# Performance work log

Measured on AMD Instinct MI355X. Metric: run time of the kernel, lower is better.

Reference implementation:

```python
import jax, jax.numpy as jnp
import numpy as np

BETA_HAT_2 = 2.0


def _forward(x, cw0, cb0, cw1, cb1, cw2, cb2,
             Wq, bq, Wk, bk, Wv, bv, Wo, bo, omega, gamma, W1, b1, W2, b2):
    # ---- conv frontal stem: (Conv1D same -> ReLU -> AvgPool(4)) x 3 ----
    def conv_relu(h, w, b):
        y = jax.lax.conv_general_dilated(h, w, window_strides=(1,), padding='SAME',
                                         dimension_numbers=('NWC', 'WIO', 'NWC'))
        return jax.nn.relu(y + b)

    def avg_pool(h, p=4):
        B, L, C = h.shape
        return h.reshape(B, L // p, p, C).mean(axis=2)

    h = avg_pool(conv_relu(x, cw0, cb0))
    h = avg_pool(conv_relu(h, cw1, cb1))
    h = avg_pool(conv_relu(h, cw2, cb2))   # [B, S, D]

    B, S, D = h.shape
    H, Dh = gamma.shape[1], omega.shape[2]
    M = 2 * omega.shape[3]                 # d_kernel_map
    inv_sqrt_m = 1.0 / np.sqrt(M)

    # ---- PositionalFeature: normalized positions x ALiBi-like slope ladder ----
    slopes = jnp.arange(D, 0, -4.0, dtype=h.dtype) / D * BETA_HAT_2   # [D/4]
    t = jnp.arange(S, dtype=h.dtype) / (S - 1)                        # [S]
    fwd = t[:, None] * slopes[None, :]                                # [S, D/4]
    pos_q = jnp.concatenate([fwd, fwd[::-1]], axis=-1)                # [S, M] (forward, backward)
    pos_k = -pos_q                                                    # (neg_forward, neg_backward)

    def lc(z):  # LayerCentering: mean-subtraction over features (no scale)
        return z - z.mean(axis=-1, keepdims=True)

    def fourier(z, om):  # z [B,S,H,Dh], om [H,Dh,M/2] -> [B,S,H,M]
        proj = jnp.einsum('bshd,hdm->bshm', z, om)
        return jnp.concatenate([jnp.cos(proj), jnp.sin(proj)], axis=-1) * inv_sqrt_m

    def layer(carry, p):
        hc = carry
        wq, bq_, wk, bk_, wv, bv_, wo, bo_, om, g, w1, b1_, w2, b2_ = p
        a_in = lc(hc)  # preLC
        q = (a_in @ wq + bq_).reshape(B, S, H, Dh)
        k = (a_in @ wk + bk_).reshape(B, S, H, Dh)
        v = (a_in @ wv + bv_).reshape(B, S, H, Dh)
        qf = fourier(q, om)
        kf = fourier(k, om)
        # factorized exponential positional modulation, per-head learnable slope g:
        # A_ij[m] ~ qf_i[m] kf_j[m] exp(g*s_m*(t_i - t_j))  (ALiBi-style, linear-time)
        eq = jnp.exp(g[None, :, None] * pos_q[:, None, :])  # [S,H,M]
        ek = jnp.exp(g[None, :, None] * pos_k[:, None, :])  # [S,H,M]
        qt = qf * eq[None]
        kt = kf * ek[None]
        kv = jnp.einsum('bshm,bshe->bhme', kt, v)            # [B,H,M,Dh]
        o = jnp.einsum('bshm,bhme->bshe', qt, kv).reshape(B, S, H * Dh)
        hc = hc + (o @ wo + bo_)                              # residual (dropout inactive)
        f_in = lc(hc)                                         # preLC before FF
        hc = hc + (jax.nn.relu(f_in @ w1 + b1_) @ w2 + b2_)   # PositionwiseFF + residual
        return hc, None

    h, _ = jax.lax.scan(layer, h, (Wq, bq, Wk, bk, Wv, bv, Wo, bo, omega, gamma, W1, b1, W2, b2))
    return h


def setup_inputs() -> dict:
    key = jax.random.key(0)
    ks = jax.random.split(key, 16)
    B, Lraw = 8, 131072
    NL, D, H, Dh, Dff, M = 2, 256, 8, 32, 1024, 128
    f32 = jnp.float32
    x = jax.random.normal(ks[0], (B, Lraw, 1), f32)

    def w(k, shape, fan_in):
        return jax.random.normal(k, shape, f32) / np.sqrt(fan_in)

    cw0 = w(ks[1], (11, 1, 8), 11 * 1)
    cw1 = w(ks[2], (3, 8, 16), 3 * 8)
    cw2 = w(ks[3], (3, 16, D), 3 * 16)
    Wq = w(ks[4], (NL, D, H * Dh), D)
    Wk = w(ks[5], (NL, D, H * Dh), D)
    Wv = w(ks[6], (NL, D, H * Dh), D)
    Wo = w(ks[7], (NL, H * Dh, D), H * Dh)
    W1 = w(ks[8], (NL, D, Dff), D)
    W2 = w(ks[9], (NL, Dff, D), Dff)
    omega = jax.random.normal(ks[10], (NL, H, Dh, M // 2), f32)  # fourier projection
    g0 = jax.random.uniform(ks[11], (1, H), f32, 0.0, 0.5)       # layer 0: head_init_range (0, 0.5)
    gr = jax.random.uniform(ks[12], (NL - 1, H), f32, 0.0, 1.0)  # others: (0, 1.0) ('forward')
    gamma = jnp.concatenate([g0, gr], axis=0)
    z = lambda *s: jnp.zeros(s, f32)
    return {"x": x, "cw0": cw0, "cb0": z(8), "cw1": cw1, "cb1": z(16), "cw2": cw2, "cb2": z(D),
            "Wq": Wq, "bq": z(NL, H * Dh), "Wk": Wk, "bk": z(NL, H * Dh), "Wv": Wv, "bv": z(NL, H * Dh),
            "Wo": Wo, "bo": z(NL, D), "omega": omega, "gamma": gamma,
            "W1": W1, "b1": z(NL, Dff), "W2": W2, "b2": z(NL, D)}


def reference(x, cw0, cb0, cw1, cb1, cw2, cb2, Wq, bq, Wk, bk, Wv, bv, Wo, bo, omega, gamma, W1, b1, W2, b2):
    return _forward(x, cw0, cb0, cw1, cb1, cw2, cb2,
                    Wq, bq, Wk, bk, Wv, bv, Wo, bo, omega, gamma, W1, b1, W2, b2)
```

## Files before the change

kernel.cpp:

```cpp
#include <hip/hip_runtime.h>
#include <hip/hip_bf16.h>
#include <math.h>

#define BATCH 8
#define LRAW 131072
#define L1P 32768
#define L2P 8192
#define SEQ 2048
#define DMODEL 256
#define NHEAD 8
#define DHEAD 32
#define MDIM 128
#define MHALF 64
#define DFF 1024
#define BS_TOK (BATCH*SEQ)
#define INV_SQRT_M 0.08838834764831845f

typedef __attribute__((ext_vector_type(8))) short s8v;
typedef __attribute__((ext_vector_type(4))) float f4v;

static __device__ __forceinline__ f4v mfma16(s8v a, s8v b, f4v c) {
    return __builtin_amdgcn_mfma_f32_16x16x32_bf16(a, b, c, 0, 0, 0);
}
static __device__ __forceinline__ unsigned short f2bf(float x) {
    __hip_bfloat16 h = __float2bfloat16(x);
    return *reinterpret_cast<unsigned short*>(&h);
}
static __device__ __forceinline__ float bf2f(unsigned short u) {
    __hip_bfloat16 h; *reinterpret_cast<unsigned short*>(&h) = u;
    return __bfloat162float(h);
}
static __device__ __forceinline__ void split8(const float* v, unsigned short* dh, unsigned short* dl) {
#pragma unroll
    for (int j = 0; j < 8; j++) {
        unsigned short hv = f2bf(v[j]);
        dh[j] = hv;
        dl[j] = f2bf(v[j] - bf2f(hv));
    }
}
static __device__ __forceinline__ void split_frag(const float* v, s8v& hi, s8v& lo) {
#pragma unroll
    for (int j = 0; j < 8; j++) {
        unsigned short hv = f2bf(v[j]);
        hi[j] = (short)hv;
        lo[j] = (short)f2bf(v[j] - bf2f(hv));
    }
}
static __device__ __forceinline__ int swz(int row, int kq) {
    return row * 32 + ((kq ^ ((row >> 1) & 3)) << 3);
}


__global__ __launch_bounds__(256) void conv0_kernel(const float* __restrict__ x,
    const float* __restrict__ w, const float* __restrict__ bias, float* __restrict__ out)
{
    int idx = blockIdx.x * 256 + threadIdx.x;
    if (idx >= BATCH * L1P) return;
    int b = idx >> 15;
    int p = idx & (L1P - 1);
    const float* xb = x + (size_t)b * LRAW;
    float acc[8];
#pragma unroll
    for (int c = 0; c < 8; c++) acc[c] = 0.f;
#pragma unroll
    for (int i = 0; i < 4; i++) {
        int base = 4 * p + i - 5;
        float y[8];
#pragma unroll
        for (int c = 0; c < 8; c++) y[c] = bias[c];
#pragma unroll
        for (int kk = 0; kk < 11; kk++) {
            int xi = base + kk;
            float xv = (xi >= 0 && xi < LRAW) ? xb[xi] : 0.f;
#pragma unroll
            for (int c = 0; c < 8; c++) y[c] = fmaf(xv, w[kk * 8 + c], y[c]);
        }
#pragma unroll
        for (int c = 0; c < 8; c++) acc[c] += fmaxf(y[c], 0.f);
    }
    float* op = out + (size_t)idx * 8;
#pragma unroll
    for (int c = 0; c < 8; c++) op[c] = acc[c] * 0.25f;
}

__global__ __launch_bounds__(256) void conv1_kernel(const float* __restrict__ in,
    const float* __restrict__ w, const float* __restrict__ bias, float* __restrict__ out)
{
    int idx = blockIdx.x * 256 + threadIdx.x;
    if (idx >= BATCH * L2P) return;
    int b = idx >> 13;
    int p = idx & (L2P - 1);
    const float* ib = in + (size_t)b * L1P * 8;
    float acc[16];
#pragma unroll
    for (int c = 0; c < 16; c++) acc[c] = 0.f;
#pragma unroll
    for (int i = 0; i < 4; i++) {
        float y[16];
#pragma unroll
        for (int c = 0; c < 16; c++) y[c] = bias[c];
#pragma unroll
        for (int kk = 0; kk < 3; kk++) {
            int pos = 4 * p + i + kk - 1;
            if (pos < 0 || pos >= L1P) continue;
            const float* row = ib + (size_t)pos * 8;
#pragma unroll
            for (int ci = 0; ci < 8; ci++) {
                float xv = row[ci];
#pragma unroll
                for (int c = 0; c < 16; c++) y[c] = fmaf(xv, w[(kk * 8 + ci) * 16 + c], y[c]);
            }
        }
#pragma unroll
        for (int c = 0; c < 16; c++) acc[c] += fmaxf(y[c], 0.f);
    }
    float* op = out + (size_t)idx * 16;
#pragma unroll
    for (int c = 0; c < 16; c++) op[c] = acc[c] * 0.25f;
}

__global__ __launch_bounds__(256) void conv2_kernel(const float* __restrict__ in,
    const float* __restrict__ w, const float* __restrict__ bias, float* __restrict__ out)
{
    int bp = blockIdx.x;
    int b = bp / SEQ, p = bp % SEQ;
    int co = threadIdx.x;
    __shared__ float win[6][16];
    int t = threadIdx.x;
    if (t < 96) {
        int r = t / 16, ci = t % 16;
        int pos = 4 * p - 1 + r;
        win[r][ci] = (pos >= 0 && pos < L2P) ? in[((size_t)b * L2P + pos) * 16 + ci] : 0.f;
    }
    __syncthreads();
    float y[4];
#pragma unroll
    for (int i = 0; i < 4; i++) y[i] = bias[co];
#pragma unroll
    for (int kk = 0; kk < 3; kk++) {
#pragma unroll
        for (int ci = 0; ci < 16; ci++) {
            float wv = w[(kk * 16 + ci) * 256 + co];
#pragma unroll
            for (int i = 0; i < 4; i++) y[i] = fmaf(win[i + kk][ci], wv, y[i]);
        }
    }
    float acc = 0.f;
#pragma unroll
    for (int i = 0; i < 4; i++) acc += fmaxf(y[i], 0.f);
    out[((size_t)b * SEQ + p) * 256 + co] = acc * 0.25f;
}


__global__ __launch_bounds__(256) void tconv4_kernel(
    const float* __restrict__ s0, const float* __restrict__ s1,
    const float* __restrict__ s2, const float* __restrict__ s3,
    unsigned short* __restrict__ dst)
{
    int z = blockIdx.z;
    const float* in = (z == 0) ? s0 : (z == 1) ? s1 : (z == 2) ? s2 : s3;
    unsigned short* outs = dst + (size_t)z * 131072;
    const int R = 256, C = 256;
    __shared__ float tile[32][33];
    int t = threadIdx.x;
    int r0 = blockIdx.y * 32, c0 = blockIdx.x * 32;
    int r = t >> 3, cq = t & 7;
    float4 v = *(const float4*)(in + (size_t)(r0 + r) * C + c0 + cq * 4);
    tile[r][cq * 4 + 0] = v.x; tile[r][cq * 4 + 1] = v.y;
    tile[r][cq * 4 + 2] = v.z; tile[r][cq * 4 + 3] = v.w;
    __syncthreads();
    ushort4 hi, lo;
    unsigned short* hp = (unsigned short*)&hi;
    unsigned short* lp = (unsigned short*)&lo;
#pragma unroll
    for (int j = 0; j < 4; j++) {
        float x = tile[cq * 4 + j][r];
        hp[j] = f2bf(x);
        lp[j] = f2bf(x - bf2f(hp[j]));
    }
    size_t ob = (size_t)(c0 + r) * (2 * R) + r0 + cq * 4;
    *(ushort4*)&outs[ob] = hi;
    *(ushort4*)&outs[ob + R] = lo;
}

__global__ __launch_bounds__(256) void tconv_ff_kernel(
    const float* __restrict__ W1_l, const float* __restrict__ W2_l,
    unsigned short* __restrict__ w1t, unsigned short* __restrict__ w2t)
{
    int z = blockIdx.z;
    int bx = z ? blockIdx.y : blockIdx.x;
    int by = z ? blockIdx.x : blockIdx.y;
    const float* in = z ? W2_l : W1_l;
    unsigned short* outs = z ? w2t : w1t;
    int R = z ? 1024 : 256;
    int C = z ? 256 : 1024;
    __shared__ float tile[32][33];
    int t = threadIdx.x;
    int r0 = by * 32, c0 = bx * 32;
    int r = t >> 3, cq = t & 7;
    float4 v = *(const float4*)(in + (size_t)(r0 + r) * C + c0 + cq * 4);
    tile[r][cq * 4 + 0] = v.x; tile[r][cq * 4 + 1] = v.y;
    tile[r][cq * 4 + 2] = v.z; tile[r][cq * 4 + 3] = v.w;
    __syncthreads();
    ushort4 hi, lo;
    unsigned short* hp = (unsigned short*)&hi;
    unsigned short* lp = (unsigned short*)&lo;
#pragma unroll
    for (int j = 0; j < 4; j++) {
        float x = tile[cq * 4 + j][r];
        hp[j] = f2bf(x);
        lp[j] = f2bf(x - bf2f(hp[j]));
    }
    size_t ob = (size_t)(c0 + r) * (2 * R) + r0 + cq * 4;
    *(ushort4*)&outs[ob] = hi;
    *(ushort4*)&outs[ob + R] = lo;
}


__global__ __launch_bounds__(256) void center_split(
    const float* __restrict__ hc, unsigned short* __restrict__ hcs)
{
    __shared__ float psum[64][4];
    __shared__ float muS[64];
    const int t = threadIdx.x;
    const int row = t >> 2, q4 = t & 3;
    const size_t grow = (size_t)blockIdx.x * 64 + row;
    const float* rp = hc + grow * DMODEL + q4 * 64;
    float4 va[16];
    float s = 0.f;
#pragma unroll
    for (int j = 0; j < 16; j++) {
        va[j] = *(const float4*)(rp + j * 4);
        s += va[j].x + va[j].y + va[j].z + va[j].w;
    }
    psum[row][q4] = s;
    __syncthreads();
    if (t < 64) muS[t] = (psum[t][0] + psum[t][1] + psum[t][2] + psum[t][3]) * (1.0f / 256.0f);
    __syncthreads();
    const float mu = muS[row];
    unsigned short* op = hcs + grow * 512 + q4 * 64;
#pragma unroll
    for (int j = 0; j < 8; j++) {
        float v[8] = {va[2*j].x - mu, va[2*j].y - mu, va[2*j].z - mu, va[2*j].w - mu,
                      va[2*j+1].x - mu, va[2*j+1].y - mu, va[2*j+1].z - mu, va[2*j+1].w - mu};
        unsigned short hb[8], lb[8];
        split8(v, hb, lb);
        *(uint4*)(op + j * 8) = *(const uint4*)hb;
        *(uint4*)(op + 256 + j * 8) = *(const uint4*)lb;
    }
}


template<bool RESID>
__global__ __launch_bounds__(256) void gemm64s(
    const unsigned short* __restrict__ Abuf, int ARS, int ALO,
    const unsigned short* __restrict__ Bbuf, int BRS, int BLO,
    const float* __restrict__ bias, const float* __restrict__ resid,
    float* __restrict__ C, int N, int K)
{
    __shared__ unsigned short AsH[64 * 32];
    __shared__ unsigned short AsL[64 * 32];
    __shared__ unsigned short BsH[64 * 32];
    __shared__ unsigned short BsL[64 * 32];
    const int t = threadIdx.x;
    const int n0 = blockIdx.y * 64, m0 = blockIdx.x * 64;
    const int row = t >> 2, kq = t & 3, seg = kq * 8;
    const int lane = t & 63, w = t >> 6;
    const int wm = w & 1, wn = w >> 1, m16 = lane & 15, q = lane >> 4;
    const f4v fz = {0.f, 0.f, 0.f, 0.f};
    f4v acc[2][2] = {{fz, fz}, {fz, fz}};
    const size_t aoff = (size_t)(m0 + row) * ARS + seg;
    const size_t boff = (size_t)(n0 + row) * BRS + seg;
    const int lw = swz(row, kq);
    for (int k0 = 0; k0 < K; k0 += 32) {
        __syncthreads();
        *(uint4*)&AsH[lw] = *(const uint4*)(Abuf + aoff + k0);
        *(uint4*)&AsL[lw] = *(const uint4*)(Abuf + aoff + ALO + k0);
        *(uint4*)&BsH[lw] = *(const uint4*)(Bbuf + boff + k0);
        *(uint4*)&BsL[lw] = *(const uint4*)(Bbuf + boff + BLO + k0);
        __syncthreads();
        s8v ah[2], al[2], bh[2], bl[2];
#pragma unroll
        for (int i = 0; i < 2; i++) {
            int ar = wm * 32 + i * 16 + m16;
            int br = wn * 32 + i * 16 + m16;
            int ro = swz(ar, q);
            int co = swz(br, q);
            ah[i] = *(const s8v*)&AsH[ro];
            al[i] = *(const s8v*)&AsL[ro];
            bh[i] = *(const s8v*)&BsH[co];
            bl[i] = *(const s8v*)&BsL[co];
        }
#pragma unroll
        for (int mt = 0; mt < 2; mt++)
#pragma unroll
            for (int nt = 0; nt < 2; nt++) {
                acc[mt][nt] = mfma16(ah[mt], bh[nt], acc[mt][nt]);
                acc[mt][nt] = mfma16(ah[mt], bl[nt], acc[mt][nt]);
                acc[mt][nt] = mfma16(al[mt], bh[nt], acc[mt][nt]);
            }
    }
#pragma unroll
    for (int mt = 0; mt < 2; mt++)
#pragma unroll
        for (int nt = 0; nt < 2; nt++)
#pragma unroll
            for (int r = 0; r < 4; r++) {
                int rg = m0 + wm * 32 + mt * 16 + q * 4 + r;
                int cg = n0 + wn * 32 + nt * 16 + m16;
                float val = acc[mt][nt][r] + bias[cg];
                if (RESID) val += resid[(size_t)rg * N + cg];
                C[(size_t)rg * N + cg] = val;
            }
}

__global__ __launch_bounds__(256) void gemm64_qkv2(
    const unsigned short* __restrict__ Abuf, const unsigned short* __restrict__ Bbuf,
    const float* __restrict__ bk, const float* __restrict__ bv, const float* __restrict__ bq,
    float* __restrict__ C)
{
    __shared__ unsigned short AsH[64 * 32];
    __shared__ unsigned short AsL[64 * 32];
    __shared__ unsigned short BsH[64 * 32];
    __shared__ unsigned short BsL[64 * 32];
    const int t = threadIdx.x;
    const int n0 = blockIdx.y * 64, m0 = blockIdx.x * 64;
    const int row = t >> 2, kq = t & 3, seg = kq * 8;
    const int lane = t & 63, w = t >> 6;
    const int wm = w & 1, wn = w >> 1, m16 = lane & 15, q = lane >> 4;
    const f4v fz = {0.f, 0.f, 0.f, 0.f};
    f4v acc[2][2] = {{fz, fz}, {fz, fz}};
    const size_t aoff = (size_t)(m0 + row) * 512 + seg;
    const size_t boff = (size_t)(n0 + row) * 512 + seg;
    const int lw = swz(row, kq);
    for (int k0 = 0; k0 < 256; k0 += 32) {
        __syncthreads();
        *(uint4*)&AsH[lw] = *(const uint4*)(Abuf + aoff + k0);
        *(uint4*)&AsL[lw] = *(const uint4*)(Abuf + aoff + 256 + k0);
        *(uint4*)&BsH[lw] = *(const uint4*)(Bbuf + boff + k0);
        *(uint4*)&BsL[lw] = *(const uint4*)(Bbuf + boff + 256 + k0);
        __syncthreads();
        s8v ah[2], al[2], bh[2], bl[2];
#pragma unroll
        for (int i = 0; i < 2; i++) {
            int ar = wm * 32 + i * 16 + m16;
            int br = wn * 32 + i * 16 + m16;
            int ro = swz(ar, q);
            int co = swz(br, q);
            ah[i] = *(const s8v*)&AsH[ro];
            al[i] = *(const s8v*)&AsL[ro];
            bh[i] = *(const s8v*)&BsH[co];
            bl[i] = *(const s8v*)&BsL[co];
        }
#pragma unroll
        for (int mt = 0; mt < 2; mt++)
#pragma unroll
            for (int nt = 0; nt < 2; nt++) {
                acc[mt][nt] = mfma16(ah[mt], bh[nt], acc[mt][nt]);
                acc[mt][nt] = mfma16(ah[mt], bl[nt], acc[mt][nt]);
                acc[mt][nt] = mfma16(al[mt], bh[nt], acc[mt][nt]);
            }
    }
    const float* bp = (n0 < 256) ? bk : (n0 < 512) ? (bv - 256) : (bq - 512);
#pragma unroll
    for (int mt = 0; mt < 2; mt++)
#pragma unroll
        for (int nt = 0; nt < 2; nt++)
#pragma unroll
            for (int r = 0; r < 4; r++) {
                int rg = m0 + wm * 32 + mt * 16 + q * 4 + r;
                int cg = n0 + wn * 32 + nt * 16 + m16;
                C[(size_t)rg * 768 + cg] = acc[mt][nt][r] + bp[cg];
            }
}

__global__ __launch_bounds__(256) void gemm128_ff1b(
    const unsigned short* __restrict__ Abuf, const unsigned short* __restrict__ Bbuf,
    const float* __restrict__ bias, unsigned short* __restrict__ Us)
{
    __shared__ unsigned short AsH[128 * 32];
    __shared__ unsigned short AsL[128 * 32];
    __shared__ unsigned short BsH[128 * 32];
    __shared__ unsigned short BsL[128 * 32];
    const int t = threadIdx.x;
    const int n0 = blockIdx.y * 128, m0 = blockIdx.x * 128;
    const int lane = t & 63, w = t >> 6;
    const int wm = w & 1, wn = w >> 1, m16 = lane & 15, q = lane >> 4;
    const f4v fz = {0.f, 0.f, 0.f, 0.f};
    f4v acc[4][4];
#pragma unroll
    for (int i = 0; i < 4; i++)
#pragma unroll
        for (int j = 0; j < 4; j++) acc[i][j] = fz;
    const int c0 = t * 2, c1 = t * 2 + 1;
    const int r0i = c0 >> 2, q0i = c0 & 3, s0i = q0i * 8;
    const int r1i = c1 >> 2, q1i = c1 & 3, s1i = q1i * 8;
    const unsigned short* a0p = Abuf + (size_t)(m0 + r0i) * 512 + s0i;
    const unsigned short* a1p = Abuf + (size_t)(m0 + r1i) * 512 + s1i;
    const size_t b0o = (size_t)(n0 + r0i) * 512 + s0i;
    const size_t b1o = (size_t)(n0 + r1i) * 512 + s1i;
    const int l0 = swz(r0i, q0i);
    const int l1 = swz(r1i, q1i);
    for (int k0 = 0; k0 < 256; k0 += 32) {
        __syncthreads();
        *(uint4*)&AsH[l0] = *(const uint4*)(a0p + k0);
        *(uint4*)&AsH[l1] = *(const uint4*)(a1p + k0);
        *(uint4*)&AsL[l0] = *(const uint4*)(a0p + 256 + k0);
        *(uint4*)&AsL[l1] = *(const uint4*)(a1p + 256 + k0);
        *(uint4*)&BsH[l0] = *(const uint4*)(Bbuf + b0o + k0);
        *(uint4*)&BsH[l1] = *(const uint4*)(Bbuf + b1o + k0);
        *(uint4*)&BsL[l0] = *(const uint4*)(Bbuf + b0o + 256 + k0);
        *(uint4*)&BsL[l1] = *(const uint4*)(Bbuf + b1o + 256 + k0);
        __syncthreads();
        s8v ah[4], al[4], bh[4], bl[4];
#pragma unroll
        for (int i = 0; i < 4; i++) {
            int ar = wm * 64 + i * 16 + m16;
            int br = wn * 64 + i * 16 + m16;
            int ro = swz(ar, q);
            int co = swz(br, q);
            ah[i] = *(const s8v*)&AsH[ro];
            al[i] = *(const s8v*)&AsL[ro];
            bh[i] = *(const s8v*)&BsH[co];
            bl[i] = *(const s8v*)&BsL[co];
        }
#pragma unroll
        for (int mt = 0; mt < 4; mt++)
#pragma unroll
            for (int nt = 0; nt < 4; nt++) {
                acc[mt][nt] = mfma16(ah[mt], bh[nt], acc[mt][nt]);
                acc[mt][nt] = mfma16(ah[mt], bl[nt], acc[mt][nt]);
                acc[mt][nt] = mfma16(al[mt], bh[nt], acc[mt][nt]);
            }
    }
#pragma unroll
    for (int mt = 0; mt < 4; mt++)
#pragma unroll
        for (int nt = 0; nt < 4; nt++)
#pragma unroll
            for (int r = 0; r < 4; r++) {
                int rg = m0 + wm * 64 + mt * 16 + q * 4 + r;
                int cg = n0 + wn * 64 + nt * 16 + m16;
                float val = fmaxf(acc[mt][nt][r] + bias[cg], 0.f);
                unsigned short hv = f2bf(val);
                Us[(size_t)rg * 2048 + cg] = hv;
                Us[(size_t)rg * 2048 + 1024 + cg] = f2bf(val - bf2f(hv));
            }
}


__global__ __launch_bounds__(256) void phi_kv_chunk(
    const float* __restrict__ qkv, const float* __restrict__ om_l,
    const float* __restrict__ g_l, float* __restrict__ part)
{
    int bx = blockIdx.x;
    int sub = bx & 15;
    int bh = bx >> 4;
    int b = bh >> 3, h = bh & 7;
    int t = threadIdx.x;
    __shared__ float omS[32][64];
    __shared__ float kS[8][32];
    __shared__ float vS[8][32];
    __shared__ float ktS[8][128];
    for (int i = t; i < 2048; i += 256) omS[i >> 6][i & 63] = om_l[(size_t)h * 2048 + i];
    float g = g_l[h];
    int e = t & 31;
    int ms = t >> 5;
    float accv[16];
#pragma unroll
    for (int i = 0; i < 16; i++) accv[i] = 0.f;
    int row0 = b * 2048 + sub * 128;
    for (int i0 = 0; i0 < 128; i0 += 8) {
        __syncthreads();
        {
            int row = row0 + i0 + ms;
            kS[ms][e] = qkv[(size_t)row * 768 + h * 32 + e];
            vS[ms][e] = qkv[(size_t)row * 768 + 256 + h * 32 + e];
        }
        __syncthreads();
        {
            int id = t * 2;
            int t2 = id >> 6;
            int mp = id & 63;
            float t_s = (float)(sub * 128 + i0 + t2) * (1.0f / 2047.0f);
#pragma unroll
            for (int u2 = 0; u2 < 2; u2++) {
                int mpp = mp + u2;
                float proj = 0.f;
#pragma unroll
                for (int d = 0; d < 32; d++) proj = fmaf(kS[t2][d], omS[d][mpp], proj);
                float slope = 2.0f - (float)mpp * 0.03125f;
                ktS[t2][mpp]      = __cosf(proj) * (INV_SQRT_M * __expf(-g * t_s * slope));
                ktS[t2][64 + mpp] = __sinf(proj) * (INV_SQRT_M * __expf(-g * (1.0f - t_s) * slope));
            }
        }
        __syncthreads();
#pragma unroll
        for (int tok = 0; tok < 8; tok++) {
            float vv = vS[tok][e];
#pragma unroll
            for (int j = 0; j < 16; j++)
                accv[j] = fmaf(ktS[tok][ms * 16 + j], vv, accv[j]);
        }
    }
    float* pp = part + (size_t)(bh * 16 + sub) * 4096;
#pragma unroll
    for (int j = 0; j < 16; j++) pp[(ms * 16 + j) * 32 + e] = accv[j];
}

__global__ __launch_bounds__(256) void kv_reduce(const float* __restrict__ part,
    float* __restrict__ kvf)
{
    int bh = blockIdx.x >> 4;
    int seg = blockIdx.x & 15;
    int i = seg * 256 + threadIdx.x;
    const float* base = part + (size_t)(bh * 16) * 4096 + i;
    float v[16];
#pragma unroll
    for (int sub = 0; sub < 16; sub++)
        v[sub] = base[(size_t)sub * 4096];
    float s = 0.f;
#pragma unroll
    for (int sub = 0; sub < 16; sub++) s += v[sub];
    kvf[(size_t)bh * 4096 + i] = s;
}

__global__ __launch_bounds__(256, 3) void phi_o_chunk(
    const float* __restrict__ qkv, const float* __restrict__ kvf,
    const float* __restrict__ om_l, const float* __restrict__ g_l,
    unsigned short* __restrict__ osplit)
{
    __shared__ unsigned short qtH[128][72];
    __shared__ unsigned short qtL[128][72];
    __shared__ unsigned short kvbH[32][72];
    __shared__ unsigned short kvbL[32][72];

    const int bx = blockIdx.x;
    const int sub = bx & 15;
    const int bh = bx >> 4;
    const int b = bh >> 3, h = bh & 7;
    const int t = threadIdx.x;
    const float g = g_l[h];
    const int row0 = b * 2048 + sub * 128;

    const int w = t >> 6, lane = t & 63, m16 = lane & 15, q = lane >> 4;
    const int tokb = w * 32;

    s8v qah[2], qal[2];
#pragma unroll
    for (int tau = 0; tau < 2; tau++) {
        const float* qp = qkv + (size_t)(row0 + tokb + tau * 16 + m16) * 768 + 512 + h * 32 + q * 8;
        float4 v0 = *(const float4*)qp;
        float4 v1 = *(const float4*)(qp + 4);
        float vv[8] = {v0.x, v0.y, v0.z, v0.w, v1.x, v1.y, v1.z, v1.w};
        split_frag(vv, qah[tau], qal[tau]);
    }

    const f4v fz = {0.f, 0.f, 0.f, 0.f};
    f4v acc[2][2] = {{fz, fz}, {fz, fz}};

    for (int p = 0; p < 2; p++) {
        if (p) __syncthreads();

#pragma unroll
        for (int vi = 0; vi < 4; vi++) {
            int pidx = t + vi * 256;
            int e = pidx & 31, j = pidx >> 5;
            float c = kvf[(size_t)bh * 4096 + (p * 32 + j) * 32 + e];
            float s = kvf[(size_t)bh * 4096 + (64 + p * 32 + j) * 32 + e];
            unsigned short ch = f2bf(c), sh = f2bf(s);
            unsigned short cl = f2bf(c - bf2f(ch)), sl = f2bf(s - bf2f(sh));
            *(unsigned*)&kvbH[e][2 * j] = (unsigned)ch | ((unsigned)sh << 16);
            *(unsigned*)&kvbL[e][2 * j] = (unsigned)cl | ((unsigned)sl << 16);
        }

        s8v obh[2], obl[2];
#pragma unroll
        for (int mu = 0; mu < 2; mu++) {
            int mh_g = p * 32 + mu * 16 + m16;
            const float* op = om_l + (size_t)h * 2048 + (q * 8) * 64 + mh_g;
            float vv[8];
#pragma unroll
            for (int jj = 0; jj < 8; jj++) vv[jj] = op[jj * 64];
            split_frag(vv, obh[mu], obl[mu]);
        }

        f4v pr[2][2] = {{fz, fz}, {fz, fz}};
#pragma unroll
        for (int tau = 0; tau < 2; tau++)
#pragma unroll
            for (int mu = 0; mu < 2; mu++) {
                pr[tau][mu] = mfma16(qah[tau], obh[mu], pr[tau][mu]);
                pr[tau][mu] = mfma16(qah[tau], obl[mu], pr[tau][mu]);
                pr[tau][mu] = mfma16(qal[tau], obh[mu], pr[tau][mu]);
            }

#pragma unroll
        for (int tau = 0; tau < 2; tau++)
#pragma unroll
            for (int mu = 0; mu < 2; mu++) {
                int mf = mu * 16 + m16;
                int mh_g = p * 32 + mf;
                float slope = 2.0f - (float)mh_g * 0.03125f;
#pragma unroll
                for (int r = 0; r < 4; r++) {
                    int tokr = tokb + tau * 16 + q * 4 + r;
                    float t_s = (float)(sub * 128 + tokr) * (1.0f / 2047.0f);
                    float proj = pr[tau][mu][r];
                    float ec = INV_SQRT_M * __expf(g * t_s * slope);
                    float es = INV_SQRT_M * __expf(g * (1.0f - t_s) * slope);
                    float bc = __cosf(proj) * ec;
                    float bs = __sinf(proj) * es;
                    unsigned short bch = f2bf(bc), bsh = f2bf(bs);
                    unsigned short bcl = f2bf(bc - bf2f(bch)), bsl = f2bf(bs - bf2f(bsh));
                    *(unsigned*)&qtH[tokr][2 * mf] = (unsigned)bch | ((unsigned)bsh << 16);
                    *(unsigned*)&qtL[tokr][2 * mf] = (unsigned)bcl | ((unsigned)bsl << 16);
                }
            }
        __syncthreads();

#pragma unroll
        for (int ks = 0; ks < 2; ks++) {
            s8v aH[2], aL[2], bH[2], bL[2];
#pragma unroll
            for (int tau = 0; tau < 2; tau++) {
                int ro = tokb + tau * 16 + m16;
                aH[tau] = *(const s8v*)&qtH[ro][ks * 32 + q * 8];
                aL[tau] = *(const s8v*)&qtL[ro][ks * 32 + q * 8];
            }
#pragma unroll
            for (int nu = 0; nu < 2; nu++) {
                int co = nu * 16 + m16;
                bH[nu] = *(const s8v*)&kvbH[co][ks * 32 + q * 8];
                bL[nu] = *(const s8v*)&kvbL[co][ks * 32 + q * 8];
            }
#pragma unroll
            for (int tau = 0; tau < 2; tau++)
#pragma unroll
                for (int nu = 0; nu < 2; nu++) {
                    acc[tau][nu] = mfma16(aH[tau], bH[nu], acc[tau][nu]);
                    acc[tau][nu] = mfma16(aH[tau], bL[nu], acc[tau][nu]);
                    acc[tau][nu] = mfma16(aL[tau], bH[nu], acc[tau][nu]);
                }
        }
    }

#pragma unroll
    for (int tau = 0; tau < 2; tau++)
#pragma unroll
        for (int nu = 0; nu < 2; nu++)
#pragma unroll
            for (int r = 0; r < 4; r++) {
                int tokr = tokb + tau * 16 + q * 4 + r;
                int e = nu * 16 + m16;
                size_t row = (size_t)(row0 + tokr);
                float val = acc[tau][nu][r];
                unsigned short hv = f2bf(val);
                osplit[row * 512 + h * 32 + e] = hv;
                osplit[row * 512 + 256 + h * 32 + e] = f2bf(val - bf2f(hv));
            }
}


extern "C" void kernel_launch(void* const* d_in, const int* in_sizes, int n_in,
                              void* d_out, int out_size, void* d_ws, size_t ws_size,
                              hipStream_t stream)
{
    (void)in_sizes; (void)n_in; (void)out_size; (void)ws_size;
    const float* x    = (const float*)d_in[0];
    const float* cw0  = (const float*)d_in[1];
    const float* cb0  = (const float*)d_in[2];
    const float* cw1  = (const float*)d_in[3];
    const float* cb1  = (const float*)d_in[4];
    const float* cw2  = (const float*)d_in[5];
    const float* cb2  = (const float*)d_in[6];
    const float* Wq   = (const float*)d_in[7];
    const float* bq   = (const float*)d_in[8];
    const float* Wk   = (const float*)d_in[9];
    const float* bk   = (const float*)d_in[10];
    const float* Wv   = (const float*)d_in[11];
    const float* bv   = (const float*)d_in[12];
    const float* Wo   = (const float*)d_in[13];
    const float* bo   = (const float*)d_in[14];
    const float* omega= (const float*)d_in[15];
    const float* gamma= (const float*)d_in[16];
    const float* W1   = (const float*)d_in[17];
    const float* b1   = (const float*)d_in[18];
    const float* W2   = (const float*)d_in[19];
    const float* b2   = (const float*)d_in[20];

    char* wsb = (char*)d_ws;
    float* hc     = (float*)wsb;
    float* qkvc   = (float*)(wsb + ((size_t)16 << 20));
    unsigned short* osplit = (unsigned short*)(wsb + ((size_t)64 << 20));
    float* part   = (float*)(wsb + ((size_t)80 << 20));
    float* kvfinal= (float*)(wsb + ((size_t)96 << 20));
    unsigned short* wqkvt = (unsigned short*)(wsb + ((size_t)97 << 20));
    unsigned short* wot   = wqkvt + 3 * 131072;
    unsigned short* w1t   = (unsigned short*)(wsb + ((size_t)98 << 20));
    unsigned short* w2t   = w1t + 524288;
    unsigned short* usp   = (unsigned short*)(wsb + ((size_t)100 << 20));
    unsigned short* hcs   = (unsigned short*)(wsb + ((size_t)164 << 20));

    char* dob = (char*)d_out;
    float* h0 = (float*)dob;
    float* h1 = (float*)(dob + ((size_t)8 << 20));

    conv0_kernel<<<(BATCH * L1P + 255) / 256, 256, 0, stream>>>(x, cw0, cb0, h0);
    conv1_kernel<<<(BATCH * L2P + 255) / 256, 256, 0, stream>>>(h0, cw1, cb1, h1);
    conv2_kernel<<<BATCH * SEQ, 256, 0, stream>>>(h1, cw2, cb2, hc);

    for (int l = 0; l < 2; l++) {
        const float* Wq_l = Wq + (size_t)l * DMODEL * DMODEL;
        const float* bq_l = bq + (size_t)l * DMODEL;
        const float* Wk_l = Wk + (size_t)l * DMODEL * DMODEL;
        const float* bk_l = bk + (size_t)l * DMODEL;
        const float* Wv_l = Wv + (size_t)l * DMODEL * DMODEL;
        const float* bv_l = bv + (size_t)l * DMODEL;
        const float* Wo_l = Wo + (size_t)l * DMODEL * DMODEL;
        const float* bo_l = bo + (size_t)l * DMODEL;
        const float* om_l = omega + (size_t)l * NHEAD * DHEAD * MHALF;
        const float* g_l  = gamma + (size_t)l * NHEAD;
        const float* W1_l = W1 + (size_t)l * DMODEL * DFF;
        const float* b1_l = b1 + (size_t)l * DFF;
        const float* W2_l = W2 + (size_t)l * DFF * DMODEL;
        const float* b2_l = b2 + (size_t)l * DMODEL;

        tconv4_kernel<<<dim3(8, 8, 4), 256, 0, stream>>>(Wk_l, Wv_l, Wq_l, Wo_l, wqkvt);
        center_split<<<BS_TOK / 64, 256, 0, stream>>>(hc, hcs);
        gemm64_qkv2<<<dim3(BS_TOK / 64, 12), 256, 0, stream>>>(
            hcs, wqkvt, bk_l, bv_l, bq_l, qkvc);
        phi_kv_chunk<<<1024, 256, 0, stream>>>(qkvc, om_l, g_l, part);
        kv_reduce<<<1024, 256, 0, stream>>>(part, kvfinal);
        phi_o_chunk<<<1024, 256, 0, stream>>>(qkvc, kvfinal, om_l, g_l, osplit);
        gemm64s<true><<<dim3(BS_TOK / 64, 4), 256, 0, stream>>>(
            osplit, 512, 256, wot, 512, 256, bo_l, hc, hc, DMODEL, DMODEL);

        tconv_ff_kernel<<<dim3(32, 8, 2), 256, 0, stream>>>(W1_l, W2_l, w1t, w2t);
        center_split<<<BS_TOK / 64, 256, 0, stream>>>(hc, hcs);
        gemm128_ff1b<<<dim3(BS_TOK / 128, DFF / 128), 256, 0, stream>>>(
            hcs, w1t, b1_l, usp);
        float* dest = (l == 1) ? (float*)d_out : hc;
        gemm64s<true><<<dim3(BS_TOK / 64, 4), 256, 0, stream>>>(
            usp, 2048, 1024, w2t, 2048, 1024, b2_l, hc, dest, DMODEL, DFF);
    }
}
```

Before: 598.1 us.

## Compute phi_kv chunk projections and KV outer products with split-bf16 MFMA

Rewrites the phi_kv_chunk kernel so that both the omega projection of K and the feature-by-V accumulation run on MFMA 16x16x32 bf16 instructions instead of scalar FMAs. To keep roughly fp32 accuracy it uses a hi/lo bf16 split with three MFMAs per product. It processes 32 tokens per step with transposed LDS tiles, padded to stride 40 to reduce bank conflicts. This cuts FP32 ALU work and the number of sync rounds, at the cost of split/convert overhead and slight precision loss from dropping the lo*lo term.

```diff
diff --git a/kernel.cpp b/kernel.cpp
--- a/kernel.cpp
+++ b/kernel.cpp
@@ -453,59 +453,116 @@
     const float* __restrict__ qkv, const float* __restrict__ om_l,
     const float* __restrict__ g_l, float* __restrict__ part)
 {
-    int bx = blockIdx.x;
-    int sub = bx & 15;
-    int bh = bx >> 4;
-    int b = bh >> 3, h = bh & 7;
-    int t = threadIdx.x;
-    __shared__ float omS[32][64];
-    __shared__ float kS[8][32];
-    __shared__ float vS[8][32];
-    __shared__ float ktS[8][128];
-    for (int i = t; i < 2048; i += 256) omS[i >> 6][i & 63] = om_l[(size_t)h * 2048 + i];
-    float g = g_l[h];
-    int e = t & 31;
-    int ms = t >> 5;
-    float accv[16];
-#pragma unroll
-    for (int i = 0; i < 16; i++) accv[i] = 0.f;
-    int row0 = b * 2048 + sub * 128;
-    for (int i0 = 0; i0 < 128; i0 += 8) {
+    __shared__ unsigned short ktTH[128 * 40];
+    __shared__ unsigned short ktTL[128 * 40];
+    __shared__ unsigned short vTH[32 * 40];
+    __shared__ unsigned short vTL[32 * 40];
+
+    const int bx = blockIdx.x;
+    const int sub = bx & 15;
+    const int bh = bx >> 4;
+    const int b = bh >> 3, h = bh & 7;
+    const int t = threadIdx.x;
+    const float g = g_l[h];
+    const int row0 = b * 2048 + sub * 128;
+
+    const int w = t >> 6, lane = t & 63, m16 = lane & 15, q = lane >> 4;
+    const int mh = w * 16 + m16;
+    const int ve = t & 31, vtq = t >> 5;
+
+    s8v obh, obl;
+    {
+        const float* op = om_l + (size_t)h * 2048 + (q * 8) * 64 + mh;
+        float vv[8];
+#pragma unroll
+        for (int jj = 0; jj < 8; jj++) vv[jj] = op[jj * 64];
+        split_frag(vv, obh, obl);
+    }
+    const float slope = 2.0f - (float)mh * 0.03125f;
+
+    const f4v fz = {0.f, 0.f, 0.f, 0.f};
+    f4v acc[2][2] = {{fz, fz}, {fz, fz}};
+
+    for (int step = 0; step < 4; step++) {
+        if (step) __syncthreads();
+
+#pragma unroll
+        for (int j = 0; j < 4; j++) {
+            int tok = vtq + 8 * j;
+            float v = qkv[(size_t)(row0 + step * 32 + tok) * 768 + 256 + h * 32 + ve];
+            unsigned short hv = f2bf(v);
+            vTH[ve * 40 + tok] = hv;
+            vTL[ve * 40 + tok] = f2bf(v - bf2f(hv));
+        }
+
+        f4v pr[2] = {fz, fz};
+#pragma unroll
+        for (int tau = 0; tau < 2; tau++) {
+            const float* kp = qkv + (size_t)(row0 + step * 32 + tau * 16 + m16) * 768 + h * 32 + q * 8;
+            float4 v0 = *(const float4*)kp;
+            float4 v1 = *(const float4*)(kp + 4);
+            float vv[8] = {v0.x, v0.y, v0.z, v0.w, v1.x, v1.y, v1.z, v1.w};
+            s8v kah, kal;
+            split_frag(vv, kah, kal);
+            pr[tau] = mfma16(kah, obh, pr[tau]);
+            pr[tau] = mfma16(kah, obl, pr[tau]);
+            pr[tau] = mfma16(kal, obh, pr[tau]);
+        }
+
+#pragma unroll
+        for (int tau = 0; tau < 2; tau++)
+#pragma unroll
+            for (int r = 0; r < 4; r++) {
+                int tokl = tau * 16 + q * 4 + r;
+                float t_s = (float)(sub * 128 + step * 32 + tokl) * (1.0f / 2047.0f);
+                float proj = pr[tau][r];
+                float ec = INV_SQRT_M * __expf(-g * t_s * slope);
+                float es = INV_SQRT_M * __expf(-g * (1.0f - t_s) * slope);
+                float bc = __cosf(proj) * ec;
+                float bs = __sinf(proj) * es;
+                unsigned short bch = f2bf(bc), bsh = f2bf(bs);
+                unsigned short bcl = f2bf(bc - bf2f(bch)), bsl = f2bf(bs - bf2f(bsh));
+                ktTH[mh * 40 + tokl] = bch;
+                ktTL[mh * 40 + tokl] = bcl;
+                ktTH[(64 + mh) * 40 + tokl] = bsh;
+                ktTL[(64 + mh) * 40 + tokl] = bsl;
+            }
         __syncthreads();
-        {
-            int row = row0 + i0 + ms;
-            kS[ms][e] = qkv[(size_t)row * 768 + h * 32 + e];
-            vS[ms][e] = qkv[(size_t)row * 768 + 256 + h * 32 + e];
-        }
-        __syncthreads();
-        {
-            int id = t * 2;
-            int t2 = id >> 6;
-            int mp = id & 63;
-            float t_s = (float)(sub * 128 + i0 + t2) * (1.0f / 2047.0f);
-#pragma unroll
-            for (int u2 = 0; u2 < 2; u2++) {
-                int mpp = mp + u2;
-                float proj = 0.f;
-#pragma unroll
-                for (int d = 0; d < 32; d++) proj = fmaf(kS[t2][d], omS[d][mpp], proj);
-                float slope = 2.0f - (float)mpp * 0.03125f;
-                ktS[t2][mpp]      = __cosf(proj) * (INV_SQRT_M * __expf(-g * t_s * slope));
-                ktS[t2][64 + mpp] = __sinf(proj) * (INV_SQRT_M * __expf(-g * (1.0f - t_s) * slope));
-            }
-        }
-        __syncthreads();
-#pragma unroll
-        for (int tok = 0; tok < 8; tok++) {
-            float vv = vS[tok][e];
-#pragma unroll
-            for (int j = 0; j < 16; j++)
-                accv[j] = fmaf(ktS[tok][ms * 16 + j], vv, accv[j]);
-        }
-    }
+
+        s8v aH[2], aL[2], bH[2], bL[2];
+#pragma unroll
+        for (int tau = 0; tau < 2; tau++) {
+            int ro = (w * 32 + tau * 16 + m16) * 40 + q * 8;
+            aH[tau] = *(const s8v*)&ktTH[ro];
+            aL[tau] = *(const s8v*)&ktTL[ro];
+        }
+#pragma unroll
+        for (int nu = 0; nu < 2; nu++) {
+            int co = (nu * 16 + m16) * 40 + q * 8;
+            bH[nu] = *(const s8v*)&vTH[co];
+            bL[nu] = *(const s8v*)&vTL[co];
+        }
+#pragma unroll
+        for (int tau = 0; tau < 2; tau++)
+#pragma unroll
+            for (int nu = 0; nu < 2; nu++) {
+                acc[tau][nu] = mfma16(aH[tau], bH[nu], acc[tau][nu]);
+                acc[tau][nu] = mfma16(aH[tau], bL[nu], acc[tau][nu]);
+                acc[tau][nu] = mfma16(aL[tau], bH[nu], acc[tau][nu]);
+            }
+    }
+
     float* pp = part + (size_t)(bh * 16 + sub) * 4096;
 #pragma unroll
-    for (int j = 0; j < 16; j++) pp[(ms * 16 + j) * 32 + e] = accv[j];
+    for (int tau = 0; tau < 2; tau++)
+#pragma unroll
+        for (int nu = 0; nu < 2; nu++)
+#pragma unroll
+            for (int r = 0; r < 4; r++) {
+                int m = w * 32 + tau * 16 + q * 4 + r;
+                int e = nu * 16 + m16;
+                pp[m * 32 + e] = acc[tau][nu][r];
+            }
 }
 
 __global__ __launch_bounds__(256) void kv_reduce(const float* __restrict__ part,
```

Measured after the change: 558.8 us. 6.6% less time.
